# Kernel tuning notes

Hardware: AMD Instinct MI355X
Metric: run time of the kernel (lower is better)

## Reference

```python
import jax, jax.numpy as jnp
import numpy as np

K = 7          # kernel_size
PAD = 3        # padding = (K - 1) // 2, stride = 1
H, W = 2048, 2048


def _design_pinv():
    # Same design matrix as the torch module: plane z = C0*x + C1*y + C2
    half = (K - 1) / 2
    space = np.arange(-half, half + 1, 1)
    X, Y = np.meshgrid(space, space)              # 'xy' indexing, matches np.meshgrid default
    A = np.c_[X.flatten(), Y.flatten(), np.ones(K * K)].astype(np.float32)  # [K*K, 3]
    # lstsq with full-column-rank A == pinv(A) @ v
    return jnp.asarray(np.linalg.pinv(A).astype(np.float32))  # [3, K*K]


def setup_inputs() -> dict:
    key = jax.random.key(0)
    x = jax.random.normal(key, (H, W), dtype=jnp.float32)
    return {"x": x}


def reference(x):
    h, w = x.shape
    # ReplicationPad2d == edge padding
    xp = jnp.pad(x, PAD, mode='edge')[None, None]  # [1, 1, h+2P, w+2P]
    # Extract all KxK patches; with 1 input channel the K*K channel dim is
    # kernel-row-major, matching unfold(2,K,1).unfold(3,K,1).view(N, K*K).
    patches = jax.lax.conv_general_dilated_patches(
        xp, (K, K), (1, 1), 'VALID')               # [1, K*K, h, w]
    pv = patches.reshape(K * K, h * w).T            # [h*w, K*K]
    pinvA = _design_pinv()                          # [3, K*K]
    cs = pv @ pinvA.T                               # [h*w, 3] plane coeffs per pixel
    return cs.reshape(h, w, 3)
```

## Files before the change

kernel.cpp:

```cpp
#include <hip/hip_runtime.h>

#define HH 2048
#define WW 2048
#define KK 7
#define PADK 3
#define TILE 32
#define PADT 38
#define INW 40
#define INW4 (INW / 4)
#define HSW 36
#define HSW4 (HSW / 4)

typedef float v4f __attribute__((ext_vector_type(4)));

__global__ __launch_bounds__(256)
void UnfoldPlainFit_42477226558039_kernel(const float* __restrict__ x,
                                          float* __restrict__ out) {
    __shared__ float sIn[PADT][INW];
    __shared__ float sHs[PADT][HSW];
    __shared__ float sHx[PADT][HSW];

    const int bx = blockIdx.x, by = blockIdx.y;
    const int tileR = by * TILE, tileC = bx * TILE;
    const int tid = threadIdx.x;

    if (bx > 0 && bx < (WW / TILE - 1)) {
#pragma unroll 2
        for (int idx = tid; idx < PADT * INW4; idx += 256) {
            int lr = idx / INW4;
            int k  = idx - lr * INW4;
            int gr = tileR - PADK + lr;
            gr = max(0, min(HH - 1, gr));
            const v4f* src =
                reinterpret_cast<const v4f*>(x + (size_t)gr * WW + (tileC - 4)) + k;
            reinterpret_cast<v4f*>(&sIn[lr][0])[k] = *src;
        }
    } else {
        for (int idx = tid; idx < PADT * INW; idx += 256) {
            int lr = idx / INW;
            int lc = idx - lr * INW;
            int gr = max(0, min(HH - 1, tileR - PADK + lr));
            int gc = max(0, min(WW - 1, tileC - 4 + lc));
            sIn[lr][lc] = x[(size_t)gr * WW + gc];
        }
    }
    __syncthreads();

#pragma unroll 2
    for (int idx = tid; idx < PADT * 8; idx += 256) {
        int lr = idx >> 3;
        int u  = idx & 7;
        const v4f* row4 = reinterpret_cast<const v4f*>(&sIn[lr][0]);
        v4f a = row4[u], b = row4[u + 1], c = row4[u + 2];
        float w[12] = {a.x, a.y, a.z, a.w, b.x, b.y, b.z, b.w, c.x, c.y, c.z, c.w};
        v4f hs, hx;
#pragma unroll
        for (int t = 0; t < 4; ++t) {
            float s = 0.f, wx = 0.f;
#pragma unroll
            for (int m = 0; m < KK; ++m) {
                float v = w[1 + t + m];
                s += v;
                wx = fmaf((float)(m - PADK), v, wx);
            }
            hs[t] = s;
            hx[t] = wx;
        }
        reinterpret_cast<v4f*>(&sHs[lr][0])[u] = hs;
        reinterpret_cast<v4f*>(&sHx[lr][0])[u] = hx;
    }
    __syncthreads();

    const int row = tid >> 3;
    const int u   = tid & 7;
    float c0[4] = {0.f, 0.f, 0.f, 0.f};
    float c1[4] = {0.f, 0.f, 0.f, 0.f};
    float c2[4] = {0.f, 0.f, 0.f, 0.f};
#pragma unroll
    for (int i = 0; i < KK; ++i) {
        v4f hs = reinterpret_cast<const v4f*>(&sHs[row + i][0])[u];
        v4f hx = reinterpret_cast<const v4f*>(&sHx[row + i][0])[u];
        float wy = (float)(i - PADK);
#pragma unroll
        for (int t = 0; t < 4; ++t) {
            c2[t] += hs[t];
            c1[t] = fmaf(wy, hs[t], c1[t]);
            c0[t] += hx[t];
        }
    }
    const float W196 = 1.0f / 196.0f;
    const float W49  = 1.0f / 49.0f;

    float* o = out + ((size_t)(tileR + row) * WW + tileC + 4 * u) * 3;
    v4f v0 = {c0[0] * W196, c1[0] * W196, c2[0] * W49,  c0[1] * W196};
    v4f v1 = {c1[1] * W196, c2[1] * W49,  c0[2] * W196, c1[2] * W196};
    v4f v2 = {c2[2] * W49,  c0[3] * W196, c1[3] * W196, c2[3] * W49};
    v4f* o4 = reinterpret_cast<v4f*>(o);
    __builtin_nontemporal_store(v0, o4 + 0);
    __builtin_nontemporal_store(v1, o4 + 1);
    __builtin_nontemporal_store(v2, o4 + 2);
}

extern "C" void kernel_launch(void* const* d_in, const int* in_sizes, int n_in,
                              void* d_out, int out_size, void* d_ws, size_t ws_size,
                              hipStream_t stream) {
    const float* x = (const float*)d_in[0];
    float* out = (float*)d_out;
    dim3 grid(WW / TILE, HH / TILE);
    dim3 block(256);
    UnfoldPlainFit_42477226558039_kernel<<<grid, block, 0, stream>>>(x, out);
}
```

Measured before the change: 98.80 us.

## Enlarge tile to 64x64, fuse load with horizontal pass, 16 pixels per thread

New measurement: 92.36 us. -6.5%, faster.

```diff
diff --git a/kernel.cpp b/kernel.cpp
--- a/kernel.cpp
+++ b/kernel.cpp
@@ -4,19 +4,15 @@
 #define WW 2048
 #define KK 7
 #define PADK 3
-#define TILE 32
-#define PADT 38
-#define INW 40
-#define INW4 (INW / 4)
-#define HSW 36
-#define HSW4 (HSW / 4)
+#define TILE 64
+#define PADT (TILE + 6)
+#define HSW 68
 
 typedef float v4f __attribute__((ext_vector_type(4)));
 
 __global__ __launch_bounds__(256)
 void UnfoldPlainFit_42477226558039_kernel(const float* __restrict__ x,
                                           float* __restrict__ out) {
-    __shared__ float sIn[PADT][INW];
     __shared__ float sHs[PADT][HSW];
     __shared__ float sHx[PADT][HSW];
 
@@ -24,81 +20,107 @@
     const int tileR = by * TILE, tileC = bx * TILE;
     const int tid = threadIdx.x;
 
-    if (bx > 0 && bx < (WW / TILE - 1)) {
-#pragma unroll 2
-        for (int idx = tid; idx < PADT * INW4; idx += 256) {
-            int lr = idx / INW4;
-            int k  = idx - lr * INW4;
-            int gr = tileR - PADK + lr;
-            gr = max(0, min(HH - 1, gr));
-            const v4f* src =
-                reinterpret_cast<const v4f*>(x + (size_t)gr * WW + (tileC - 4)) + k;
-            reinterpret_cast<v4f*>(&sIn[lr][0])[k] = *src;
+    const bool interior = (bx > 0) & (bx < (WW / TILE - 1));
+    if (interior) {
+#pragma unroll
+        for (int it = 0; it < 5; ++it) {
+            int idx = tid + it * 256;
+            if (idx < PADT * 16) {
+                int lr = idx >> 4;
+                int u  = idx & 15;
+                int gr = max(0, min(HH - 1, tileR - PADK + lr));
+                const v4f* p = reinterpret_cast<const v4f*>(
+                    x + (size_t)gr * WW + (tileC + 4 * u - 4));
+                v4f a = p[0], b = p[1], c = p[2];
+                float w[12] = {a.x, a.y, a.z, a.w, b.x, b.y, b.z, b.w,
+                               c.x, c.y, c.z, c.w};
+                v4f hs, hx;
+#pragma unroll
+                for (int t = 0; t < 4; ++t) {
+                    float s = 0.f, wx = 0.f;
+#pragma unroll
+                    for (int m = 0; m < KK; ++m) {
+                        float v = w[1 + t + m];
+                        s += v;
+                        wx = fmaf((float)(m - PADK), v, wx);
+                    }
+                    hs[t] = s;
+                    hx[t] = wx;
+                }
+                reinterpret_cast<v4f*>(&sHs[lr][0])[u] = hs;
+                reinterpret_cast<v4f*>(&sHx[lr][0])[u] = hx;
+            }
         }
     } else {
-        for (int idx = tid; idx < PADT * INW; idx += 256) {
-            int lr = idx / INW;
-            int lc = idx - lr * INW;
+        for (int idx = tid; idx < PADT * 16; idx += 256) {
+            int lr = idx >> 4;
+            int u  = idx & 15;
             int gr = max(0, min(HH - 1, tileR - PADK + lr));
-            int gc = max(0, min(WW - 1, tileC - 4 + lc));
-            sIn[lr][lc] = x[(size_t)gr * WW + gc];
+            const float* rowp = x + (size_t)gr * WW;
+            float w[12];
+#pragma unroll
+            for (int j = 0; j < 12; ++j) {
+                int gc = max(0, min(WW - 1, tileC + 4 * u - 4 + j));
+                w[j] = rowp[gc];
+            }
+            v4f hs, hx;
+#pragma unroll
+            for (int t = 0; t < 4; ++t) {
+                float s = 0.f, wx = 0.f;
+#pragma unroll
+                for (int m = 0; m < KK; ++m) {
+                    float v = w[1 + t + m];
+                    s += v;
+                    wx = fmaf((float)(m - PADK), v, wx);
+                }
+                hs[t] = s;
+                hx[t] = wx;
+            }
+            reinterpret_cast<v4f*>(&sHs[lr][0])[u] = hs;
+            reinterpret_cast<v4f*>(&sHx[lr][0])[u] = hx;
         }
     }
     __syncthreads();
 
-#pragma unroll 2
-    for (int idx = tid; idx < PADT * 8; idx += 256) {
-        int lr = idx >> 3;
-        int u  = idx & 7;
-        const v4f* row4 = reinterpret_cast<const v4f*>(&sIn[lr][0]);
-        v4f a = row4[u], b = row4[u + 1], c = row4[u + 2];
-        float w[12] = {a.x, a.y, a.z, a.w, b.x, b.y, b.z, b.w, c.x, c.y, c.z, c.w};
-        v4f hs, hx;
+    const int row = tid >> 2;
+    const int ug  = tid & 3;
+    float c0[16], c1[16], c2[16];
 #pragma unroll
-        for (int t = 0; t < 4; ++t) {
-            float s = 0.f, wx = 0.f;
-#pragma unroll
-            for (int m = 0; m < KK; ++m) {
-                float v = w[1 + t + m];
-                s += v;
-                wx = fmaf((float)(m - PADK), v, wx);
-            }
-            hs[t] = s;
-            hx[t] = wx;
-        }
-        reinterpret_cast<v4f*>(&sHs[lr][0])[u] = hs;
-        reinterpret_cast<v4f*>(&sHx[lr][0])[u] = hx;
-    }
-    __syncthreads();
+    for (int t = 0; t < 16; ++t) { c0[t] = 0.f; c1[t] = 0.f; c2[t] = 0.f; }
 
-    const int row = tid >> 3;
-    const int u   = tid & 7;
-    float c0[4] = {0.f, 0.f, 0.f, 0.f};
-    float c1[4] = {0.f, 0.f, 0.f, 0.f};
-    float c2[4] = {0.f, 0.f, 0.f, 0.f};
 #pragma unroll
     for (int i = 0; i < KK; ++i) {
-        v4f hs = reinterpret_cast<const v4f*>(&sHs[row + i][0])[u];
-        v4f hx = reinterpret_cast<const v4f*>(&sHx[row + i][0])[u];
         float wy = (float)(i - PADK);
+        const v4f* hs4 = reinterpret_cast<const v4f*>(&sHs[row + i][0]) + 4 * ug;
+        const v4f* hx4 = reinterpret_cast<const v4f*>(&sHx[row + i][0]) + 4 * ug;
 #pragma unroll
-        for (int t = 0; t < 4; ++t) {
-            c2[t] += hs[t];
-            c1[t] = fmaf(wy, hs[t], c1[t]);
-            c0[t] += hx[t];
+        for (int j = 0; j < 4; ++j) {
+            v4f hs = hs4[j], hx = hx4[j];
+#pragma unroll
+            for (int t = 0; t < 4; ++t) {
+                int k = 4 * j + t;
+                c2[k] += hs[t];
+                c1[k] = fmaf(wy, hs[t], c1[k]);
+                c0[k] += hx[t];
+            }
         }
     }
+
     const float W196 = 1.0f / 196.0f;
     const float W49  = 1.0f / 49.0f;
 
-    float* o = out + ((size_t)(tileR + row) * WW + tileC + 4 * u) * 3;
-    v4f v0 = {c0[0] * W196, c1[0] * W196, c2[0] * W49,  c0[1] * W196};
-    v4f v1 = {c1[1] * W196, c2[1] * W49,  c0[2] * W196, c1[2] * W196};
-    v4f v2 = {c2[2] * W49,  c0[3] * W196, c1[3] * W196, c2[3] * W49};
+    float* o = out + ((size_t)(tileR + row) * WW + tileC + 16 * ug) * 3;
     v4f* o4 = reinterpret_cast<v4f*>(o);
-    __builtin_nontemporal_store(v0, o4 + 0);
-    __builtin_nontemporal_store(v1, o4 + 1);
-    __builtin_nontemporal_store(v2, o4 + 2);
+#pragma unroll
+    for (int g = 0; g < 4; ++g) {
+        int k = 4 * g;
+        v4f v0 = {c0[k+0] * W196, c1[k+0] * W196, c2[k+0] * W49,  c0[k+1] * W196};
+        v4f v1 = {c1[k+1] * W196, c2[k+1] * W49,  c0[k+2] * W196, c1[k+2] * W196};
+        v4f v2 = {c2[k+2] * W49,  c0[k+3] * W196, c1[k+3] * W196, c2[k+3] * W49};
+        o4[3 * g + 0] = v0;
+        o4[3 * g + 1] = v1;
+        o4[3 * g + 2] = v2;
+    }
 }
 
 extern "C" void kernel_launch(void* const* d_in, const int* in_sizes, int n_in,
```
